# Optimization experiments

Hardware: AMD Instinct MI355X
Metric: run time of the kernel (lower is better)

The kernel has to match this reference:

```python
import jax, jax.numpy as jnp
import numpy as np

K = 16
CIN = 128
COUT = 128
EPS = 1e-5
SLOPE = 0.01  # default negative_slope of nn.LeakyReLU


def _bn(w, gamma, beta):
    # BatchNorm1d in training mode over channel axis (last): stats over (N, k)
    mean = jnp.mean(w, axis=(0, 1))
    var = jnp.var(w, axis=(0, 1))  # biased variance, as torch uses for normalization
    return (w - mean) * jax.lax.rsqrt(var + EPS) * gamma + beta


def _leaky(x):
    return jnp.where(x >= 0, x, SLOPE * x)


def setup_inputs() -> dict:
    key = jax.random.key(0)
    ks = jax.random.split(key, 10)
    N = 8192
    s = 0.05
    return {
        "fea_i": jax.random.normal(ks[0], (N, CIN), jnp.float32),
        "fea_last": jax.random.normal(ks[1], (N, CIN), jnp.float32),
        "xyz_i": jax.random.uniform(ks[2], (N, 3), jnp.float32),
        "xyz_last": jax.random.uniform(ks[3], (N, 3), jnp.float32),
        "batch": jnp.zeros((N,), jnp.int32),
        "Wq": jax.random.normal(ks[4], (COUT, CIN), jnp.float32) * s,
        "bq": jnp.zeros((COUT,), jnp.float32),
        "Wk": jax.random.normal(ks[5], (COUT, CIN), jnp.float32) * s,
        "bk": jnp.zeros((COUT,), jnp.float32),
        "Wv": jax.random.normal(ks[6], (COUT, CIN), jnp.float32) * s,
        "bv": jnp.zeros((COUT,), jnp.float32),
        "bn1_gamma": jnp.ones((COUT,), jnp.float32),
        "bn1_beta": jnp.zeros((COUT,), jnp.float32),
        "Wl": jax.random.normal(ks[7], (COUT, COUT), jnp.float32) * s,
        "bl": jnp.zeros((COUT,), jnp.float32),
        "bn2_gamma": jnp.ones((COUT,), jnp.float32),
        "bn2_beta": jnp.zeros((COUT,), jnp.float32),
    }


def reference(fea_i, fea_last, xyz_i, xyz_last, batch, Wq, bq, Wk, bk, Wv, bv,
              bn1_gamma, bn1_beta, Wl, bl, bn2_gamma, bn2_beta):
    # knn: for each point in xyz_last, K nearest neighbors in xyz_i (single batch)
    d2 = jnp.sum((xyz_last[:, None, :] - xyz_i[None, :, :]) ** 2, axis=-1)  # (N, N)
    _, idx = jax.lax.top_k(-d2, K)  # (N, K) indices into xyz_i / fea_i

    fk = fea_i[idx]                                   # (N, K, CIN) gathered neighbor feats
    q = fea_last @ Wq.T + bq                          # (N, COUT); fea_last[idx_last] == row-repeat
    kk = jnp.einsum('nkc,oc->nko', fk, Wk) + bk       # (N, K, COUT)
    w = q[:, None, :] - kk                            # (N, K, COUT)

    # lin_w: BN -> LeakyReLU -> Linear -> BN -> LeakyReLU
    w = _leaky(_bn(w, bn1_gamma, bn1_beta))
    w = jnp.einsum('nko,po->nkp', w, Wl) + bl
    w = _leaky(_bn(w, bn2_gamma, bn2_beta))

    w = jax.nn.softmax(w, axis=1)                     # softmax over K neighbors
    v = jnp.einsum('nkc,oc->nko', fk, Wv) + bv        # (N, K, COUT)
    return jnp.sum(w * v, axis=1)                     # (N, COUT)
```

## Files before the change

### kernel.cpp

```cpp
#include <hip/hip_runtime.h>
#include <stdint.h>

#define NPTS   8192
#define NROWS  (NPTS * 16)
#define SLOPE  0.01f
#define BN_EPS 1e-5f
#define INVM   (1.f / (float)NROWS)

#define TP     0.13f
#define TP2    (TP * TP)
#define LDEP   6
#define LSTR   7
#define TF     0.2f
#define TF2    0.04f
#define CAPF   408
#define EPSB   1e-5f

#define OFF_Q      0u
#define OFF_KP     4194304u
#define OFF_VP     8388608u
#define OFF_STATS  12582912u
#define OFF_TAB    12845056u
#define OFF_IDX    13041664u
#define OFF_BIG    13585408u
#define WS_NEED    47139840u

#define T_POFF 0

typedef __bf16 bf16x8 __attribute__((ext_vector_type(8)));
typedef float  f32x4  __attribute__((ext_vector_type(4)));

__device__ __forceinline__ unsigned int pack_bf2(float lo, float hi) {
  unsigned int a = __float_as_uint(lo);
  unsigned int b = __float_as_uint(hi);
  unsigned int ra = (a + 0x7fffu + ((a >> 16) & 1u)) >> 16;
  unsigned int rb = (b + 0x7fffu + ((b >> 16) & 1u)) & 0xffff0000u;
  return ra | rb;
}
__device__ __forceinline__ unsigned short bf1(float v) {
  unsigned int a = __float_as_uint(v);
  return (unsigned short)((a + 0x7fffu + ((a >> 16) & 1u)) >> 16);
}
__device__ __forceinline__ float bf2f(unsigned short u) {
  return __uint_as_float(((unsigned int)u) << 16);
}

__device__ __forceinline__ int cell_of(float x, float y, float z) {
  int cx = min(7, max(0, (int)(x * 8.f)));
  int cy = min(7, max(0, (int)(y * 8.f)));
  int cz = min(7, max(0, (int)(z * 8.f)));
  return (cz * 8 + cy) * 8 + cx;
}

__device__ __forceinline__ void insert16(unsigned long long* key, unsigned long long kk) {
  if (kk < key[15]) {
    #pragma unroll
    for (int u = 15; u >= 1; --u) {
      bool cm1 = kk < key[u - 1];
      bool cs  = kk < key[u];
      key[u] = cm1 ? key[u - 1] : (cs ? kk : key[u]);
    }
    key[0] = (kk < key[0]) ? kk : key[0];
  }
}

template<int D>
__device__ __forceinline__ void tournament16(unsigned long long (&lst)[D], int lane,
                                             int* __restrict__ sidxq, int* __restrict__ idxoq) {
  int myidx = 0;
  #pragma unroll 1
  for (int r = 0; r < 16; ++r) {
    const float hd = __uint_as_float((unsigned int)(lst[0] >> 32));
    float wm = hd;
    #pragma unroll
    for (int o = 32; o; o >>= 1) wm = fminf(wm, __shfl_xor(wm, o));
    bool iswin = (hd == wm);
    const unsigned long long wmask = __ballot(iswin);
    unsigned int widx;
    if (__popcll(wmask) > 1) {
      unsigned int mi = iswin ? (unsigned int)lst[0] : 0xffffffffu;
      #pragma unroll
      for (int o = 32; o; o >>= 1) {
        unsigned int u = (unsigned int)__shfl_xor((int)mi, o);
        mi = (u < mi) ? u : mi;
      }
      widx = mi;
      iswin = iswin && ((unsigned int)lst[0] == mi);
    } else {
      const int wl = (int)__builtin_ctzll(wmask);
      widx = (unsigned int)__builtin_amdgcn_readlane((int)(unsigned int)lst[0], wl);
    }
    #pragma unroll
    for (int u = 0; u < D - 1; ++u) lst[u] = iswin ? lst[u + 1] : lst[u];
    lst[D - 1] = iswin ? ~0ull : lst[D - 1];
    if (lane == r) myidx = (int)widx;
  }
  if (lane < 16) { idxoq[lane] = myidx; sidxq[lane] = myidx; }
}

template<int D>
__device__ __forceinline__ void extract_topk(const unsigned long long* __restrict__ poolq, int n, int lane,
                                             int* __restrict__ sidxq, int* __restrict__ idxoq) {
  unsigned long long lst[D];
  #pragma unroll
  for (int j = 0; j < D; ++j) lst[j] = ~0ull;
  for (int j = lane; j < n; j += 64) {
    unsigned long long kk = poolq[j];
    #pragma unroll
    for (int u = D - 1; u >= 1; --u) {
      bool cm1 = kk < lst[u - 1];
      bool cs  = kk < lst[u];
      lst[u] = cm1 ? lst[u - 1] : (cs ? kk : lst[u]);
    }
    lst[0] = (kk < lst[0]) ? kk : lst[0];
  }
  tournament16<D>(lst, lane, sidxq, idxoq);
}

__device__ __forceinline__ int scan_ball(const int* __restrict__ poff, const float4* __restrict__ bp,
                                         float qx, float qy, float qz, float rad, float r2, int cap,
                                         unsigned long long* __restrict__ poolw,
                                         int lane, unsigned long long below) {
  const int lx = max(0, (int)floorf((qx - rad - EPSB) * 8.f));
  const int hx = min(7, (int)floorf((qx + rad + EPSB) * 8.f));
  const int ly = max(0, (int)floorf((qy - rad - EPSB) * 8.f));
  const int hy = min(7, (int)floorf((qy + rad + EPSB) * 8.f));
  const int lz = max(0, (int)floorf((qz - rad - EPSB) * 8.f));
  const int hz = min(7, (int)floorf((qz + rad + EPSB) * 8.f));
  const int nrY = hy - ly + 1, nrows = nrY * (hz - lz + 1);
  int zi = 0;
  #pragma unroll
  for (int z2 = 1; z2 < 5; ++z2) zi += (lane >= z2 * nrY) ? 1 : 0;
  const int yi = lane - zi * nrY;
  int rs = 0, re = 0;
  if (lane < nrows) {
    const int crow = ((lz + zi) * 8 + (ly + yi)) * 8;
    rs = poff[crow + lx]; re = poff[crow + hx + 1];
  }
  int cnt = 0;
  for (int r = 0; r < nrows; ++r) {
    const int rsr = __builtin_amdgcn_readlane(rs, r);
    const int rer = __builtin_amdgcn_readlane(re, r);
    for (int base = rsr; base < rer; base += 64) {
      const int pos = base + lane;
      const float4 pp = bp[pos];
      float dx = qx - pp.x, dy = qy - pp.y, dz = qz - pp.z;
      float dd = fmaf(dx, dx, fmaf(dy, dy, dz * dz));
      bool g = (pos < rer) && (dd < r2);
      unsigned long long mask = __ballot(g);
      int p2 = cnt + (int)__popcll(mask & below);
      if (g && p2 < cap)
        poolw[p2] = ((unsigned long long)__float_as_uint(dd) << 32) | (unsigned int)__float_as_int(pp.w);
      cnt += (int)__popcll(mask);
    }
  }
  return cnt;
}

__global__ __launch_bounds__(1024) void k_bin(const float* __restrict__ xyz_i,
                                              int* __restrict__ tab,
                                              float* __restrict__ stats,
                                              float4* __restrict__ bp) {
  __shared__ int cnt[512];
  __shared__ int scn[512];
  const int t = threadIdx.x;
  #pragma unroll
  for (int i = 0; i < 8; ++i) stats[i * 1024 + t] = 0.f;
  if (t < 512) cnt[t] = 0;
  if (t < 64)  bp[NPTS + t] = make_float4(1e9f, 1e9f, 1e9f, __int_as_float(0));
  __syncthreads();

  float xs[8], ys[8], zs[8]; int cl[8];
  #pragma unroll
  for (int i = 0; i < 8; ++i) {
    const int p = i * 1024 + t;
    xs[i] = xyz_i[p * 3]; ys[i] = xyz_i[p * 3 + 1]; zs[i] = xyz_i[p * 3 + 2];
    cl[i] = cell_of(xs[i], ys[i], zs[i]);
    atomicAdd(&cnt[cl[i]], 1);
  }
  __syncthreads();

  if (t < 512) scn[t] = cnt[t];
  __syncthreads();
  for (int ofs = 1; ofs < 512; ofs <<= 1) {
    int add = (t < 512 && t >= ofs) ? scn[t - ofs] : 0;
    __syncthreads();
    if (t < 512) scn[t] += add;
    __syncthreads();
  }
  if (t < 512) tab[T_POFF + t] = scn[t] - cnt[t];
  if (t == 511) tab[T_POFF + 512] = scn[511];
  __syncthreads();
  if (t < 512) scn[t] -= cnt[t];
  __syncthreads();

  #pragma unroll
  for (int i = 0; i < 8; ++i) {
    const int pos = atomicAdd(&scn[cl[i]], 1);
    bp[pos] = make_float4(xs[i], ys[i], zs[i], __int_as_float(i * 1024 + t));
  }
}

__global__ __launch_bounds__(256) void k_proj(const float* __restrict__ fea_i,
                                              const float* __restrict__ fea_last,
                                              const float* __restrict__ Wq,
                                              const float* __restrict__ Wk,
                                              const float* __restrict__ Wv,
                                              const float* __restrict__ bq,
                                              const float* __restrict__ bk,
                                              const float* __restrict__ bv,
                                              float* __restrict__ Qo,
                                              float* __restrict__ Kpo,
                                              float* __restrict__ Vpo) {
  const int z = blockIdx.y;
  const float* A    = (z == 0) ? fea_last : fea_i;
  const float* W    = (z == 0) ? Wq : ((z == 1) ? Wk : Wv);
  const float* bias = (z == 0) ? bq : ((z == 1) ? bk : bv);
  float* Out        = (z == 0) ? Qo : ((z == 1) ? Kpo : Vpo);

  __shared__ unsigned short wl[128 * 128];
  const int t = threadIdx.x;
  const int lane = t & 63, w = t >> 6;

  #pragma unroll
  for (int i = 0; i < 8; ++i) {
    const int chunk = i * 256 + t;
    const int p = chunk >> 4, cseg = chunk & 15;
    const float4 wa = *(const float4*)(W + (size_t)p * 128 + cseg * 8);
    const float4 wb = *(const float4*)(W + (size_t)p * 128 + cseg * 8 + 4);
    uint4 pk;
    pk.x = pack_bf2(wa.x, wa.y); pk.y = pack_bf2(wa.z, wa.w);
    pk.z = pack_bf2(wb.x, wb.y); pk.w = pack_bf2(wb.z, wb.w);
    *(uint4*)((char*)wl + p * 256 + ((cseg * 16) ^ ((p & 7) << 4))) = pk;
  }
  __syncthreads();

  const int rowtile = blockIdx.x * 64 + w * 16;
  const int kslot = lane & 15, kgrp = lane >> 4;
  const float* Arow = A + (size_t)(rowtile + kslot) * 128;

  f32x4 acc[8];
  #pragma unroll
  for (int tt = 0; tt < 8; ++tt) acc[tt] = (f32x4){0.f, 0.f, 0.f, 0.f};

  #pragma unroll
  for (int s = 0; s < 4; ++s) {
    const int c0 = s * 32 + kgrp * 8;
    const float4 qa = *(const float4*)(Arow + c0);
    const float4 qb = *(const float4*)(Arow + c0 + 4);
    uint4 af;
    af.x = pack_bf2(qa.x, qa.y); af.y = pack_bf2(qa.z, qa.w);
    af.z = pack_bf2(qb.x, qb.y); af.w = pack_bf2(qb.z, qb.w);
    const bf16x8 Af = __builtin_bit_cast(bf16x8, af);
    const int cbyte = s * 64 + kgrp * 16;
    #pragma unroll
    for (int tt = 0; tt < 8; ++tt) {
      const int prow = tt * 16 + kslot;
      const uint4 bw = *(const uint4*)((const char*)wl + prow * 256 + (cbyte ^ ((prow & 7) << 4)));
      acc[tt] = __builtin_amdgcn_mfma_f32_16x16x32_bf16(Af, __builtin_bit_cast(bf16x8, bw), acc[tt], 0, 0, 0);
    }
  }

  #pragma unroll
  for (int tt = 0; tt < 8; ++tt) {
    const int col = tt * 16 + kslot;
    const float bb = bias[col];
    #pragma unroll
    for (int r = 0; r < 4; ++r) {
      const int row = rowtile + kgrp * 4 + r;
      Out[(size_t)row * 128 + col] = acc[tt][r] + bb;
    }
  }
}

__global__ __launch_bounds__(256) void k_knn(const int* __restrict__ tab,
                                             const float4* __restrict__ bp,
                                             const float* __restrict__ xyz_last,
                                             const float* __restrict__ Q,
                                             const float* __restrict__ Kp,
                                             int* __restrict__ idxo,
                                             float* __restrict__ st1) {
  __shared__ unsigned long long pool[4][64 * LSTR];
  __shared__ int sidx[4][16];
  __shared__ float red[4][256];
  const int t = threadIdx.x, lane = t & 63, wave = t >> 6;
  const int q = blockIdx.x * 4 + wave;
  const float qx = xyz_last[q * 3];
  const float qy = xyz_last[q * 3 + 1];
  const float qz = xyz_last[q * 3 + 2];
  const int* poff = &tab[T_POFF];
  const unsigned long long below = (1ull << lane) - 1ull;

  unsigned long long* myslots = &pool[wave][lane * LSTR];
  int cnt = 0;
  {
    const int lx = max(0, (int)floorf((qx - TP - EPSB) * 8.f));
    const int hx = min(7, (int)floorf((qx + TP + EPSB) * 8.f));
    const int ly = max(0, (int)floorf((qy - TP - EPSB) * 8.f));
    const int hy = min(7, (int)floorf((qy + TP + EPSB) * 8.f));
    const int lz = max(0, (int)floorf((qz - TP - EPSB) * 8.f));
    const int hz = min(7, (int)floorf((qz + TP + EPSB) * 8.f));
    const int nrY = hy - ly + 1, nrows = nrY * (hz - lz + 1);
    int zi = 0;
    #pragma unroll
    for (int z2 = 1; z2 < 5; ++z2) zi += (lane >= z2 * nrY) ? 1 : 0;
    const int yi = lane - zi * nrY;
    int rs = 0, re = 0;
    if (lane < nrows) {
      const int crow = ((lz + zi) * 8 + (ly + yi)) * 8;
      rs = poff[crow + lx]; re = poff[crow + hx + 1];
    }
    for (int r = 0; r < nrows; ++r) {
      const int rsr = __builtin_amdgcn_readlane(rs, r);
      const int rer = __builtin_amdgcn_readlane(re, r);
      #pragma unroll 2
      for (int base = rsr; base < rer; base += 64) {
        const int pos = base + lane;
        const float4 pp = bp[pos];
        float dx = qx - pp.x, dy = qy - pp.y, dz = qz - pp.z;
        float dd = fmaf(dx, dx, fmaf(dy, dy, dz * dz));
        if ((pos < rer) && (dd < TP2)) {
          if (cnt < LDEP)
            myslots[cnt] = ((unsigned long long)__float_as_uint(dd) << 32) | (unsigned int)__float_as_int(pp.w);
          ++cnt;
        }
      }
    }
  }
  const bool anyover = __ballot(cnt > LDEP) != 0ull;
  int tot = cnt;
  #pragma unroll
  for (int o = 32; o; o >>= 1) tot += __shfl_xor(tot, o);

  if (!anyover && tot >= 16) {
    unsigned long long lst[LDEP];
    #pragma unroll
    for (int j = 0; j < LDEP; ++j) lst[j] = ~0ull;
    for (int j = 0; j < cnt; ++j) {
      unsigned long long kk = myslots[j];
      #pragma unroll
      for (int u = LDEP - 1; u >= 1; --u) {
        bool cm1 = kk < lst[u - 1];
        bool cs  = kk < lst[u];
        lst[u] = cm1 ? lst[u - 1] : (cs ? kk : lst[u]);
      }
      lst[0] = (kk < lst[0]) ? kk : lst[0];
    }
    tournament16<LDEP>(lst, lane, &sidx[wave][0], &idxo[q * 16]);
  } else {
    unsigned long long* flat = &pool[wave][0];
    int c1 = scan_ball(poff, bp, qx, qy, qz, TF, TF2, CAPF, flat, lane, below);
    if (c1 >= 16 && c1 <= CAPF) {
      extract_topk<7>(flat, c1, lane, &sidx[wave][0], &idxo[q * 16]);
    } else {
      unsigned long long key[16];
      #pragma unroll
      for (int u = 0; u < 16; ++u) key[u] = ~0ull;
      for (int it = 0; it < NPTS / 64; ++it) {
        const float4 pp = bp[it * 64 + lane];
        float dx = qx - pp.x, dy = qy - pp.y, dz = qz - pp.z;
        float dd = fmaf(dx, dx, fmaf(dy, dy, dz * dz));
        insert16(key, ((unsigned long long)__float_as_uint(dd) << 32) | (unsigned int)__float_as_int(pp.w));
      }
      unsigned long long myout = ~0ull;
      #pragma unroll 1
      for (int r = 0; r < 16; ++r) {
        unsigned long long w = key[0];
        #pragma unroll
        for (int o = 32; o; o >>= 1) {
          unsigned long long u = __shfl_xor(w, o);
          w = (u < w) ? u : w;
        }
        if (key[0] == w) {
          #pragma unroll
          for (int u = 0; u < 15; ++u) key[u] = key[u + 1];
          key[15] = ~0ull;
        }
        if (lane == r) myout = w;
      }
      if (lane < 16) {
        idxo[q * 16 + lane] = (int)(myout & 0xffffffffull);
        sidx[wave][lane] = (int)(myout & 0xffffffffull);
      }
    }
  }

  const int c0 = lane * 2;
  const float2 qv = *(const float2*)(Q + (size_t)q * 128 + c0);
  float s0 = 0.f, s1 = 0.f, v0 = 0.f, v1 = 0.f;
  #pragma unroll 4
  for (int k = 0; k < 16; ++k) {
    const int pid = sidx[wave][k];
    const float2 kv = *(const float2*)(Kp + (size_t)pid * 128 + c0);
    const float w0 = qv.x - kv.x, w1 = qv.y - kv.y;
    s0 += w0; v0 += w0 * w0;
    s1 += w1; v1 += w1 * w1;
  }
  red[wave][c0]       = s0;  red[wave][c0 + 1]   = s1;
  red[wave][128 + c0] = v0;  red[wave][129 + c0] = v1;
  __syncthreads();
  {
    const float totv = red[0][t & 255] + red[1][t & 255] + red[2][t & 255] + red[3][t & 255];
    atomicAdd(&st1[(blockIdx.x & 15) * 256 + (t & 255)], totv);
  }
}

__global__ __launch_bounds__(256) void k_mid(const float* __restrict__ Q,
                                             const float* __restrict__ Kp,
                                             const int* __restrict__ idx,
                                             const float* __restrict__ Wl,
                                             const float* __restrict__ bl,
                                             const float* __restrict__ st1,
                                             const float* __restrict__ g1,
                                             const float* __restrict__ b1,
                                             float* __restrict__ stats2,
                                             unsigned short* __restrict__ Y) {
  __shared__ union {
    unsigned short wl[128 * 128];
    struct {
      unsigned short stage[64][136];
      float red[4 * 256];
    } ep;
  } sm;
  __shared__ float bn1s[256];

  const int t = threadIdx.x;
  const int lane = t & 63, w = t >> 6;
  const int rowbase = blockIdx.x * 64;

  #pragma unroll
  for (int i = 0; i < 8; ++i) {
    const int chunk = i * 256 + t;
    const int p = chunk >> 4, cseg = chunk & 15;
    const float4 wa = *(const float4*)(Wl + (size_t)p * 128 + cseg * 8);
    const float4 wb = *(const float4*)(Wl + (size_t)p * 128 + cseg * 8 + 4);
    uint4 pk;
    pk.x = pack_bf2(wa.x, wa.y); pk.y = pack_bf2(wa.z, wa.w);
    pk.z = pack_bf2(wb.x, wb.y); pk.w = pack_bf2(wb.z, wb.w);
    *(uint4*)((char*)sm.wl + p * 256 + ((cseg * 16) ^ ((p & 7) << 4))) = pk;
  }
  if (t < 128) {
    float s = 0.f, q2 = 0.f;
    #pragma unroll
    for (int r = 0; r < 16; ++r) { s += st1[r * 256 + t]; q2 += st1[r * 256 + 128 + t]; }
    const float mean = s * INVM;
    const float var  = fmaf(-mean, mean, q2 * INVM);
    const float sc = g1[t] * rsqrtf(var + BN_EPS);
    bn1s[t]       = sc;
    bn1s[128 + t] = fmaf(-mean, sc, b1[t]);
  }
  __syncthreads();

  const int n = blockIdx.x * 4 + w;
  const int kslot = lane & 15;
  const int kgrp  = lane >> 4;
  const int pid = idx[n * 16 + kslot];
  const float* Qrow = Q + (size_t)n * 128;
  const float* Krow = Kp + (size_t)pid * 128;

  f32x4 acc[8];
  #pragma unroll
  for (int tt = 0; tt < 8; ++tt) acc[tt] = (f32x4){0.f, 0.f, 0.f, 0.f};

  #pragma unroll
  for (int s = 0; s < 4; ++s) {
    const int c0 = s * 32 + kgrp * 8;
    const float4 qa = *(const float4*)(Qrow + c0);
    const float4 qb = *(const float4*)(Qrow + c0 + 4);
    const float4 ka = *(const float4*)(Krow + c0);
    const float4 kb = *(const float4*)(Krow + c0 + 4);
    const float4 sa = *(const float4*)(bn1s + c0);
    const float4 sb = *(const float4*)(bn1s + c0 + 4);
    const float4 ha = *(const float4*)(bn1s + 128 + c0);
    const float4 hb = *(const float4*)(bn1s + 128 + c0 + 4);
    float x[8];
    x[0] = fmaf(qa.x - ka.x, sa.x, ha.x);
    x[1] = fmaf(qa.y - ka.y, sa.y, ha.y);
    x[2] = fmaf(qa.z - ka.z, sa.z, ha.z);
    x[3] = fmaf(qa.w - ka.w, sa.w, ha.w);
    x[4] = fmaf(qb.x - kb.x, sb.x, hb.x);
    x[5] = fmaf(qb.y - kb.y, sb.y, hb.y);
    x[6] = fmaf(qb.z - kb.z, sb.z, hb.z);
    x[7] = fmaf(qb.w - kb.w, sb.w, hb.w);
    uint4 af;
    af.x = pack_bf2(fmaxf(x[0], SLOPE * x[0]), fmaxf(x[1], SLOPE * x[1]));
    af.y = pack_bf2(fmaxf(x[2], SLOPE * x[2]), fmaxf(x[3], SLOPE * x[3]));
    af.z = pack_bf2(fmaxf(x[4], SLOPE * x[4]), fmaxf(x[5], SLOPE * x[5]));
    af.w = pack_bf2(fmaxf(x[6], SLOPE * x[6]), fmaxf(x[7], SLOPE * x[7]));
    const bf16x8 A = __builtin_bit_cast(bf16x8, af);
    const int cbyte = s * 64 + kgrp * 16;
    #pragma unroll
    for (int tt = 0; tt < 8; ++tt) {
      const int prow = tt * 16 + kslot;
      const uint4 bw = *(const uint4*)((const char*)sm.wl + prow * 256 + (cbyte ^ ((prow & 7) << 4)));
      acc[tt] = __builtin_amdgcn_mfma_f32_16x16x32_bf16(A, __builtin_bit_cast(bf16x8, bw), acc[tt], 0, 0, 0);
    }
  }
  __syncthreads();

  #pragma unroll
  for (int tt = 0; tt < 8; ++tt) {
    const int col = tt * 16 + kslot;
    const float bb = bl[col];
    float s = 0.f, q2 = 0.f;
    #pragma unroll
    for (int r = 0; r < 4; ++r) {
      const float v = acc[tt][r] + bb;
      s += v; q2 += v * v;
      sm.ep.stage[w * 16 + kgrp * 4 + r][col] = bf1(v);
    }
    s  += __shfl_xor(s, 16);  s  += __shfl_xor(s, 32);
    q2 += __shfl_xor(q2, 16); q2 += __shfl_xor(q2, 32);
    if (kgrp == 0) {
      sm.ep.red[w * 256 + col]       = s;
      sm.ep.red[w * 256 + 128 + col] = q2;
    }
  }
  __syncthreads();

  #pragma unroll
  for (int i = 0; i < 4; ++i) {
    const int chunk = i * 256 + t;
    const int row = chunk >> 4, cc = chunk & 15;
    const uint4 v = *(const uint4*)&sm.ep.stage[row][cc * 8];
    *(uint4*)&Y[(size_t)(rowbase + row) * 128 + cc * 8] = v;
  }
  {
    const float tot = sm.ep.red[t] + sm.ep.red[256 + t] + sm.ep.red[512 + t] + sm.ep.red[768 + t];
    atomicAdd(&stats2[(blockIdx.x & 15) * 256 + t], tot);
  }
}

__global__ __launch_bounds__(128) void k_epi(const unsigned short* __restrict__ Y,
                                             const float* __restrict__ Vp,
                                             const int* __restrict__ idx,
                                             const float* __restrict__ st2,
                                             const float* __restrict__ g2,
                                             const float* __restrict__ b2,
                                             float* __restrict__ out) {
  const int n = blockIdx.x;
  const int p = threadIdx.x;
  float s = 0.f, q2 = 0.f;
  #pragma unroll
  for (int r = 0; r < 16; ++r) { s += st2[r * 256 + p]; q2 += st2[r * 256 + 128 + p]; }
  const float mean = s * INVM;
  const float var  = fmaf(-mean, mean, q2 * INVM);
  const float s2 = g2[p] * rsqrtf(var + BN_EPS);
  const float sh2 = fmaf(-mean, s2, b2[p]);

  float z[16];
  #pragma unroll
  for (int k = 0; k < 16; ++k) {
    float yv = bf2f(Y[(size_t)(n * 16 + k) * 128 + p]);
    float v = fmaf(yv, s2, sh2);
    z[k] = (v >= 0.f) ? v : SLOPE * v;
  }
  float m = z[0];
  #pragma unroll
  for (int k = 1; k < 16; ++k) m = fmaxf(m, z[k]);
  float acc = 0.f, denom = 0.f;
  #pragma unroll
  for (int k = 0; k < 16; ++k) {
    float e = __expf(z[k] - m);
    denom += e;
    const int pid = idx[n * 16 + k];
    acc = fmaf(e, Vp[(size_t)pid * 128 + p], acc);
  }
  out[(size_t)n * 128 + p] = acc / denom;
}

extern "C" void kernel_launch(void* const* d_in, const int* in_sizes, int n_in,
                              void* d_out, int out_size, void* d_ws, size_t ws_size,
                              hipStream_t stream) {
  const float* fea_i    = (const float*)d_in[0];
  const float* fea_last = (const float*)d_in[1];
  const float* xyz_i    = (const float*)d_in[2];
  const float* xyz_last = (const float*)d_in[3];
  const float* Wq = (const float*)d_in[5];
  const float* bq = (const float*)d_in[6];
  const float* Wk = (const float*)d_in[7];
  const float* bk = (const float*)d_in[8];
  const float* Wv = (const float*)d_in[9];
  const float* bv = (const float*)d_in[10];
  const float* g1 = (const float*)d_in[11];
  const float* b1 = (const float*)d_in[12];
  const float* Wl = (const float*)d_in[13];
  const float* bl = (const float*)d_in[14];
  const float* g2 = (const float*)d_in[15];
  const float* b2 = (const float*)d_in[16];

  if (ws_size < (size_t)WS_NEED) return;

  char* ws = (char*)d_ws;
  float*  Q      = (float*)(ws + OFF_Q);
  float*  Kp     = (float*)(ws + OFF_KP);
  float*  Vp     = (float*)(ws + OFF_VP);
  int*    tab    = (int*)  (ws + OFF_TAB);
  int*    idxb   = (int*)  (ws + OFF_IDX);
  float*  st1    = (float*)(ws + OFF_STATS);
  float*  st2    = st1 + 4096;
  float4* bp     = (float4*)(ws + OFF_BIG);
  unsigned short* Y = (unsigned short*)(ws + OFF_BIG);

  k_bin<<<1, 1024, 0, stream>>>(xyz_i, tab, st1, bp);
  k_proj<<<dim3(128, 3), 256, 0, stream>>>(fea_i, fea_last, Wq, Wk, Wv, bq, bk, bv, Q, Kp, Vp);
  k_knn<<<2048, 256, 0, stream>>>(tab, bp, xyz_last, Q, Kp, idxb, st1);
  k_mid<<<2048, 256, 0, stream>>>(Q, Kp, idxb, Wl, bl, st1, g1, b1, st2, Y);
  k_epi<<<8192, 128, 0, stream>>>(Y, Vp, idxb, st2, g2, b2, (float*)d_out);
}
```

Measured before the change: 104.3 us.

## Recompute Linear in output kernel instead of storing Y; fold binning into projection

The second-layer activations Y are no longer written to and re-read from global memory. A stats-only pass computes BN2 statistics, then a fused output kernel recomputes the MFMA Linear, applies BN2, LeakyReLU and the softmax-weighted V sum in one launch. The single-block binning kernel is also merged into the projection launch as an extra grid row, removing one launch and letting it overlap with the GEMMs. In exchange the Linear matmul and K gather run twice, and the binning block now uses 256 threads instead of 1024, which could lengthen the critical path of that grid.

Result: slower. 114.4 us (+9.7%).

```diff
diff --git a/kernel.cpp b/kernel.cpp
--- a/kernel.cpp
+++ b/kernel.cpp
@@ -36,13 +36,6 @@
   unsigned int ra = (a + 0x7fffu + ((a >> 16) & 1u)) >> 16;
   unsigned int rb = (b + 0x7fffu + ((b >> 16) & 1u)) & 0xffff0000u;
   return ra | rb;
-}
-__device__ __forceinline__ unsigned short bf1(float v) {
-  unsigned int a = __float_as_uint(v);
-  return (unsigned short)((a + 0x7fffu + ((a >> 16) & 1u)) >> 16);
-}
-__device__ __forceinline__ float bf2f(unsigned short u) {
-  return __uint_as_float(((unsigned int)u) << 16);
 }
 
 __device__ __forceinline__ int cell_of(float x, float y, float z) {
@@ -157,50 +150,6 @@
   return cnt;
 }
 
-__global__ __launch_bounds__(1024) void k_bin(const float* __restrict__ xyz_i,
-                                              int* __restrict__ tab,
-                                              float* __restrict__ stats,
-                                              float4* __restrict__ bp) {
-  __shared__ int cnt[512];
-  __shared__ int scn[512];
-  const int t = threadIdx.x;
-  #pragma unroll
-  for (int i = 0; i < 8; ++i) stats[i * 1024 + t] = 0.f;
-  if (t < 512) cnt[t] = 0;
-  if (t < 64)  bp[NPTS + t] = make_float4(1e9f, 1e9f, 1e9f, __int_as_float(0));
-  __syncthreads();
-
-  float xs[8], ys[8], zs[8]; int cl[8];
-  #pragma unroll
-  for (int i = 0; i < 8; ++i) {
-    const int p = i * 1024 + t;
-    xs[i] = xyz_i[p * 3]; ys[i] = xyz_i[p * 3 + 1]; zs[i] = xyz_i[p * 3 + 2];
-    cl[i] = cell_of(xs[i], ys[i], zs[i]);
-    atomicAdd(&cnt[cl[i]], 1);
-  }
-  __syncthreads();
-
-  if (t < 512) scn[t] = cnt[t];
-  __syncthreads();
-  for (int ofs = 1; ofs < 512; ofs <<= 1) {
-    int add = (t < 512 && t >= ofs) ? scn[t - ofs] : 0;
-    __syncthreads();
-    if (t < 512) scn[t] += add;
-    __syncthreads();
-  }
-  if (t < 512) tab[T_POFF + t] = scn[t] - cnt[t];
-  if (t == 511) tab[T_POFF + 512] = scn[511];
-  __syncthreads();
-  if (t < 512) scn[t] -= cnt[t];
-  __syncthreads();
-
-  #pragma unroll
-  for (int i = 0; i < 8; ++i) {
-    const int pos = atomicAdd(&scn[cl[i]], 1);
-    bp[pos] = make_float4(xs[i], ys[i], zs[i], __int_as_float(i * 1024 + t));
-  }
-}
-
 __global__ __launch_bounds__(256) void k_proj(const float* __restrict__ fea_i,
                                               const float* __restrict__ fea_last,
                                               const float* __restrict__ Wq,
@@ -209,17 +158,62 @@
                                               const float* __restrict__ bq,
                                               const float* __restrict__ bk,
                                               const float* __restrict__ bv,
+                                              const float* __restrict__ xyz_i,
+                                              int* __restrict__ tab,
+                                              float* __restrict__ stats,
+                                              float4* __restrict__ bp,
                                               float* __restrict__ Qo,
                                               float* __restrict__ Kpo,
                                               float* __restrict__ Vpo) {
+  __shared__ unsigned short wl[128 * 128];
+  const int t = threadIdx.x;
+
+  if (blockIdx.y == 3) {
+    if (blockIdx.x != 0) return;
+    int* cnt = (int*)wl;
+    int* sa  = cnt + 512;
+    int* sb  = sa + 512;
+    #pragma unroll
+    for (int i = 0; i < 32; ++i) stats[i * 256 + t] = 0.f;
+    cnt[t] = 0; cnt[t + 256] = 0;
+    if (t < 64) bp[NPTS + t] = make_float4(1e9f, 1e9f, 1e9f, __int_as_float(0));
+    __syncthreads();
+    #pragma unroll 4
+    for (int i = 0; i < 32; ++i) {
+      const int p = i * 256 + t;
+      atomicAdd(&cnt[cell_of(xyz_i[p * 3], xyz_i[p * 3 + 1], xyz_i[p * 3 + 2])], 1);
+    }
+    __syncthreads();
+    sa[t] = cnt[t]; sa[t + 256] = cnt[t + 256];
+    __syncthreads();
+    for (int ofs = 1; ofs < 512; ofs <<= 1) {
+      const int p1 = t + 256;
+      const int v0 = sa[t]  + ((t  >= ofs) ? sa[t  - ofs] : 0);
+      const int v1 = sa[p1] + ((p1 >= ofs) ? sa[p1 - ofs] : 0);
+      __syncthreads();
+      sa[t] = v0; sa[p1] = v1;
+      __syncthreads();
+    }
+    tab[T_POFF + t]       = sa[t]       - cnt[t];
+    tab[T_POFF + 256 + t] = sa[256 + t] - cnt[256 + t];
+    if (t == 255) tab[T_POFF + 512] = sa[511];
+    sb[t] = sa[t] - cnt[t]; sb[t + 256] = sa[256 + t] - cnt[256 + t];
+    __syncthreads();
+    #pragma unroll 4
+    for (int i = 0; i < 32; ++i) {
+      const int p = i * 256 + t;
+      const float x = xyz_i[p * 3], y = xyz_i[p * 3 + 1], z = xyz_i[p * 3 + 2];
+      const int pos = atomicAdd(&sb[cell_of(x, y, z)], 1);
+      bp[pos] = make_float4(x, y, z, __int_as_float(p));
+    }
+    return;
+  }
+
   const int z = blockIdx.y;
   const float* A    = (z == 0) ? fea_last : fea_i;
   const float* W    = (z == 0) ? Wq : ((z == 1) ? Wk : Wv);
   const float* bias = (z == 0) ? bq : ((z == 1) ? bk : bv);
   float* Out        = (z == 0) ? Qo : ((z == 1) ? Kpo : Vpo);
-
-  __shared__ unsigned short wl[128 * 128];
-  const int t = threadIdx.x;
   const int lane = t & 63, w = t >> 6;
 
   #pragma unroll
@@ -405,7 +399,116 @@
   }
 }
 
-__global__ __launch_bounds__(256) void k_mid(const float* __restrict__ Q,
+#define MID_CORE(Q_, Kp_, idx_, Wl_, st1_, g1_, b1_, wlbuf, bn1buf, accv)                        \
+  {                                                                                              \
+    _Pragma("unroll")                                                                            \
+    for (int i = 0; i < 8; ++i) {                                                                \
+      const int chunk = i * 256 + t;                                                             \
+      const int p = chunk >> 4, cseg = chunk & 15;                                               \
+      const float4 wa = *(const float4*)(Wl_ + (size_t)p * 128 + cseg * 8);                      \
+      const float4 wb = *(const float4*)(Wl_ + (size_t)p * 128 + cseg * 8 + 4);                  \
+      uint4 pk;                                                                                  \
+      pk.x = pack_bf2(wa.x, wa.y); pk.y = pack_bf2(wa.z, wa.w);                                  \
+      pk.z = pack_bf2(wb.x, wb.y); pk.w = pack_bf2(wb.z, wb.w);                                  \
+      *(uint4*)((char*)wlbuf + p * 256 + ((cseg * 16) ^ ((p & 7) << 4))) = pk;                   \
+    }                                                                                            \
+    if (t < 128) {                                                                               \
+      float s = 0.f, q2 = 0.f;                                                                   \
+      _Pragma("unroll")                                                                          \
+      for (int r = 0; r < 16; ++r) { s += st1_[r * 256 + t]; q2 += st1_[r * 256 + 128 + t]; }    \
+      const float mean = s * INVM;                                                               \
+      const float var  = fmaf(-mean, mean, q2 * INVM);                                           \
+      const float sc = g1_[t] * rsqrtf(var + BN_EPS);                                            \
+      bn1buf[t]       = sc;                                                                      \
+      bn1buf[128 + t] = fmaf(-mean, sc, b1_[t]);                                                 \
+    }                                                                                            \
+    __syncthreads();                                                                             \
+    const int pidA = idx_[n * 16 + kslot];                                                       \
+    const float* Qrow = Q_ + (size_t)n * 128;                                                    \
+    const float* Krow = Kp_ + (size_t)pidA * 128;                                                \
+    _Pragma("unroll")                                                                            \
+    for (int s = 0; s < 4; ++s) {                                                                \
+      const int c0 = s * 32 + kgrp * 8;                                                          \
+      const float4 qa = *(const float4*)(Qrow + c0);                                             \
+      const float4 qb = *(const float4*)(Qrow + c0 + 4);                                         \
+      const float4 ka = *(const float4*)(Krow + c0);                                             \
+      const float4 kb = *(const float4*)(Krow + c0 + 4);                                         \
+      const float4 sa = *(const float4*)(bn1buf + c0);                                           \
+      const float4 sb = *(const float4*)(bn1buf + c0 + 4);                                       \
+      const float4 ha = *(const float4*)(bn1buf + 128 + c0);                                     \
+      const float4 hb = *(const float4*)(bn1buf + 128 + c0 + 4);                                 \
+      float x[8];                                                                                \
+      x[0] = fmaf(qa.x - ka.x, sa.x, ha.x);                                                      \
+      x[1] = fmaf(qa.y - ka.y, sa.y, ha.y);                                                      \
+      x[2] = fmaf(qa.z - ka.z, sa.z, ha.z);                                                      \
+      x[3] = fmaf(qa.w - ka.w, sa.w, ha.w);                                                      \
+      x[4] = fmaf(qb.x - kb.x, sb.x, hb.x);                                                      \
+      x[5] = fmaf(qb.y - kb.y, sb.y, hb.y);                                                      \
+      x[6] = fmaf(qb.z - kb.z, sb.z, hb.z);                                                      \
+      x[7] = fmaf(qb.w - kb.w, sb.w, hb.w);                                                      \
+      uint4 af;                                                                                  \
+      af.x = pack_bf2(fmaxf(x[0], SLOPE * x[0]), fmaxf(x[1], SLOPE * x[1]));                     \
+      af.y = pack_bf2(fmaxf(x[2], SLOPE * x[2]), fmaxf(x[3], SLOPE * x[3]));                     \
+      af.z = pack_bf2(fmaxf(x[4], SLOPE * x[4]), fmaxf(x[5], SLOPE * x[5]));                     \
+      af.w = pack_bf2(fmaxf(x[6], SLOPE * x[6]), fmaxf(x[7], SLOPE * x[7]));                     \
+      const bf16x8 Aa = __builtin_bit_cast(bf16x8, af);                                          \
+      const int cbyte = s * 64 + kgrp * 16;                                                      \
+      _Pragma("unroll")                                                                          \
+      for (int tt = 0; tt < 8; ++tt) {                                                           \
+        const int prow = tt * 16 + kslot;                                                        \
+        const uint4 bw = *(const uint4*)((const char*)wlbuf + prow * 256 + (cbyte ^ ((prow & 7) << 4))); \
+        accv[tt] = __builtin_amdgcn_mfma_f32_16x16x32_bf16(Aa, __builtin_bit_cast(bf16x8, bw), accv[tt], 0, 0, 0); \
+      }                                                                                          \
+    }                                                                                            \
+  }
+
+__global__ __launch_bounds__(256) void k_stat2(const float* __restrict__ Q,
+                                               const float* __restrict__ Kp,
+                                               const int* __restrict__ idx,
+                                               const float* __restrict__ Wl,
+                                               const float* __restrict__ bl,
+                                               const float* __restrict__ st1,
+                                               const float* __restrict__ g1,
+                                               const float* __restrict__ b1,
+                                               float* __restrict__ st2) {
+  __shared__ unsigned short wl[128 * 128];
+  __shared__ float bn1s[256];
+  __shared__ float red[4 * 256];
+  const int t = threadIdx.x;
+  const int lane = t & 63, w = t >> 6;
+  const int n = blockIdx.x * 4 + w;
+  const int kslot = lane & 15, kgrp = lane >> 4;
+
+  f32x4 acc[8];
+  #pragma unroll
+  for (int tt = 0; tt < 8; ++tt) acc[tt] = (f32x4){0.f, 0.f, 0.f, 0.f};
+  MID_CORE(Q, Kp, idx, Wl, st1, g1, b1, wl, bn1s, acc)
+
+  #pragma unroll
+  for (int tt = 0; tt < 8; ++tt) {
+    const int col = tt * 16 + kslot;
+    const float bb = bl[col];
+    float s = 0.f, q2 = 0.f;
+    #pragma unroll
+    for (int r = 0; r < 4; ++r) {
+      const float v = acc[tt][r] + bb;
+      s += v; q2 += v * v;
+    }
+    s  += __shfl_xor(s, 16);  s  += __shfl_xor(s, 32);
+    q2 += __shfl_xor(q2, 16); q2 += __shfl_xor(q2, 32);
+    if (kgrp == 0) {
+      red[w * 256 + col]       = s;
+      red[w * 256 + 128 + col] = q2;
+    }
+  }
+  __syncthreads();
+  {
+    const float tot = red[t] + red[256 + t] + red[512 + t] + red[768 + t];
+    atomicAdd(&st2[(blockIdx.x & 15) * 256 + t], tot);
+  }
+}
+
+__global__ __launch_bounds__(256) void k_out(const float* __restrict__ Q,
                                              const float* __restrict__ Kp,
                                              const int* __restrict__ idx,
                                              const float* __restrict__ Wl,
@@ -413,160 +516,71 @@
                                              const float* __restrict__ st1,
                                              const float* __restrict__ g1,
                                              const float* __restrict__ b1,
-                                             float* __restrict__ stats2,
-                                             unsigned short* __restrict__ Y) {
-  __shared__ union {
-    unsigned short wl[128 * 128];
-    struct {
-      unsigned short stage[64][136];
-      float red[4 * 256];
-    } ep;
-  } sm;
+                                             const float* __restrict__ st2,
+                                             const float* __restrict__ g2,
+                                             const float* __restrict__ b2,
+                                             const float* __restrict__ Vp,
+                                             float* __restrict__ out) {
+  __shared__ unsigned short wl[128 * 128];
   __shared__ float bn1s[256];
-
+  __shared__ float bn2s[256];
+  __shared__ float ostage[512];
   const int t = threadIdx.x;
   const int lane = t & 63, w = t >> 6;
-  const int rowbase = blockIdx.x * 64;
-
-  #pragma unroll
-  for (int i = 0; i < 8; ++i) {
-    const int chunk = i * 256 + t;
-    const int p = chunk >> 4, cseg = chunk & 15;
-    const float4 wa = *(const float4*)(Wl + (size_t)p * 128 + cseg * 8);
-    const float4 wb = *(const float4*)(Wl + (size_t)p * 128 + cseg * 8 + 4);
-    uint4 pk;
-    pk.x = pack_bf2(wa.x, wa.y); pk.y = pack_bf2(wa.z, wa.w);
-    pk.z = pack_bf2(wb.x, wb.y); pk.w = pack_bf2(wb.z, wb.w);
-    *(uint4*)((char*)sm.wl + p * 256 + ((cseg * 16) ^ ((p & 7) << 4))) = pk;
-  }
-  if (t < 128) {
+  const int n = blockIdx.x * 4 + w;
+  const int kslot = lane & 15, kgrp = lane >> 4;
+
+  if (t >= 128 && t < 256) {
+    const int o = t - 128;
     float s = 0.f, q2 = 0.f;
     #pragma unroll
-    for (int r = 0; r < 16; ++r) { s += st1[r * 256 + t]; q2 += st1[r * 256 + 128 + t]; }
+    for (int r = 0; r < 16; ++r) { s += st2[r * 256 + o]; q2 += st2[r * 256 + 128 + o]; }
     const float mean = s * INVM;
     const float var  = fmaf(-mean, mean, q2 * INVM);
-    const float sc = g1[t] * rsqrtf(var + BN_EPS);
-    bn1s[t]       = sc;
-    bn1s[128 + t] = fmaf(-mean, sc, b1[t]);
-  }
-  __syncthreads();
-
-  const int n = blockIdx.x * 4 + w;
-  const int kslot = lane & 15;
-  const int kgrp  = lane >> 4;
-  const int pid = idx[n * 16 + kslot];
-  const float* Qrow = Q + (size_t)n * 128;
-  const float* Krow = Kp + (size_t)pid * 128;
+    const float sc = g2[o] * rsqrtf(var + BN_EPS);
+    bn2s[o]       = sc;
+    bn2s[128 + o] = fmaf(-mean, sc, b2[o]);
+  }
 
   f32x4 acc[8];
   #pragma unroll
   for (int tt = 0; tt < 8; ++tt) acc[tt] = (f32x4){0.f, 0.f, 0.f, 0.f};
-
-  #pragma unroll
-  for (int s = 0; s < 4; ++s) {
-    const int c0 = s * 32 + kgrp * 8;
-    const float4 qa = *(const float4*)(Qrow + c0);
-    const float4 qb = *(const float4*)(Qrow + c0 + 4);
-    const float4 ka = *(const float4*)(Krow + c0);
-    const float4 kb = *(const float4*)(Krow + c0 + 4);
-    const float4 sa = *(const float4*)(bn1s + c0);
-    const float4 sb = *(const float4*)(bn1s + c0 + 4);
-    const float4 ha = *(const float4*)(bn1s + 128 + c0);
-    const float4 hb = *(const float4*)(bn1s + 128 + c0 + 4);
-    float x[8];
-    x[0] = fmaf(qa.x - ka.x, sa.x, ha.x);
-    x[1] = fmaf(qa.y - ka.y, sa.y, ha.y);
-    x[2] = fmaf(qa.z - ka.z, sa.z, ha.z);
-    x[3] = fmaf(qa.w - ka.w, sa.w, ha.w);
-    x[4] = fmaf(qb.x - kb.x, sb.x, hb.x);
-    x[5] = fmaf(qb.y - kb.y, sb.y, hb.y);
-    x[6] = fmaf(qb.z - kb.z, sb.z, hb.z);
-    x[7] = fmaf(qb.w - kb.w, sb.w, hb.w);
-    uint4 af;
-    af.x = pack_bf2(fmaxf(x[0], SLOPE * x[0]), fmaxf(x[1], SLOPE * x[1]));
-    af.y = pack_bf2(fmaxf(x[2], SLOPE * x[2]), fmaxf(x[3], SLOPE * x[3]));
-    af.z = pack_bf2(fmaxf(x[4], SLOPE * x[4]), fmaxf(x[5], SLOPE * x[5]));
-    af.w = pack_bf2(fmaxf(x[6], SLOPE * x[6]), fmaxf(x[7], SLOPE * x[7]));
-    const bf16x8 A = __builtin_bit_cast(bf16x8, af);
-    const int cbyte = s * 64 + kgrp * 16;
-    #pragma unroll
-    for (int tt = 0; tt < 8; ++tt) {
-      const int prow = tt * 16 + kslot;
-      const uint4 bw = *(const uint4*)((const char*)sm.wl + prow * 256 + (cbyte ^ ((prow & 7) << 4)));
-      acc[tt] = __builtin_amdgcn_mfma_f32_16x16x32_bf16(A, __builtin_bit_cast(bf16x8, bw), acc[tt], 0, 0, 0);
-    }
-  }
-  __syncthreads();
+  MID_CORE(Q, Kp, idx, Wl, st1, g1, b1, wl, bn1s, acc)
+
+  int pid4[4];
+  #pragma unroll
+  for (int r = 0; r < 4; ++r) pid4[r] = idx[n * 16 + kgrp * 4 + r];
 
   #pragma unroll
   for (int tt = 0; tt < 8; ++tt) {
     const int col = tt * 16 + kslot;
     const float bb = bl[col];
-    float s = 0.f, q2 = 0.f;
+    const float s2v = bn2s[col], sh2v = bn2s[128 + col];
+    float zv[4];
     #pragma unroll
     for (int r = 0; r < 4; ++r) {
-      const float v = acc[tt][r] + bb;
-      s += v; q2 += v * v;
-      sm.ep.stage[w * 16 + kgrp * 4 + r][col] = bf1(v);
-    }
-    s  += __shfl_xor(s, 16);  s  += __shfl_xor(s, 32);
-    q2 += __shfl_xor(q2, 16); q2 += __shfl_xor(q2, 32);
-    if (kgrp == 0) {
-      sm.ep.red[w * 256 + col]       = s;
-      sm.ep.red[w * 256 + 128 + col] = q2;
-    }
+      const float y = fmaf(acc[tt][r] + bb, s2v, sh2v);
+      zv[r] = (y >= 0.f) ? y : SLOPE * y;
+    }
+    float m = fmaxf(fmaxf(zv[0], zv[1]), fmaxf(zv[2], zv[3]));
+    m = fmaxf(m, __shfl_xor(m, 16));
+    m = fmaxf(m, __shfl_xor(m, 32));
+    float d = 0.f, va = 0.f;
+    #pragma unroll
+    for (int r = 0; r < 4; ++r) {
+      const float e = __expf(zv[r] - m);
+      d += e;
+      va = fmaf(e, Vp[(size_t)pid4[r] * 128 + col], va);
+    }
+    d  += __shfl_xor(d, 16);  d  += __shfl_xor(d, 32);
+    va += __shfl_xor(va, 16); va += __shfl_xor(va, 32);
+    if (kgrp == 0) ostage[w * 128 + col] = va / d;
   }
   __syncthreads();
-
-  #pragma unroll
-  for (int i = 0; i < 4; ++i) {
-    const int chunk = i * 256 + t;
-    const int row = chunk >> 4, cc = chunk & 15;
-    const uint4 v = *(const uint4*)&sm.ep.stage[row][cc * 8];
-    *(uint4*)&Y[(size_t)(rowbase + row) * 128 + cc * 8] = v;
-  }
   {
-    const float tot = sm.ep.red[t] + sm.ep.red[256 + t] + sm.ep.red[512 + t] + sm.ep.red[768 + t];
-    atomicAdd(&stats2[(blockIdx.x & 15) * 256 + t], tot);
-  }
-}
-
-__global__ __launch_bounds__(128) void k_epi(const unsigned short* __restrict__ Y,
-                                             const float* __restrict__ Vp,
-                                             const int* __restrict__ idx,
-                                             const float* __restrict__ st2,
-                                             const float* __restrict__ g2,
-                                             const float* __restrict__ b2,
-                                             float* __restrict__ out) {
-  const int n = blockIdx.x;
-  const int p = threadIdx.x;
-  float s = 0.f, q2 = 0.f;
-  #pragma unroll
-  for (int r = 0; r < 16; ++r) { s += st2[r * 256 + p]; q2 += st2[r * 256 + 128 + p]; }
-  const float mean = s * INVM;
-  const float var  = fmaf(-mean, mean, q2 * INVM);
-  const float s2 = g2[p] * rsqrtf(var + BN_EPS);
-  const float sh2 = fmaf(-mean, s2, b2[p]);
-
-  float z[16];
-  #pragma unroll
-  for (int k = 0; k < 16; ++k) {
-    float yv = bf2f(Y[(size_t)(n * 16 + k) * 128 + p]);
-    float v = fmaf(yv, s2, sh2);
-    z[k] = (v >= 0.f) ? v : SLOPE * v;
-  }
-  float m = z[0];
-  #pragma unroll
-  for (int k = 1; k < 16; ++k) m = fmaxf(m, z[k]);
-  float acc = 0.f, denom = 0.f;
-  #pragma unroll
-  for (int k = 0; k < 16; ++k) {
-    float e = __expf(z[k] - m);
-    denom += e;
-    const int pid = idx[n * 16 + k];
-    acc = fmaf(e, Vp[(size_t)pid * 128 + p], acc);
-  }
-  out[(size_t)n * 128 + p] = acc / denom;
+    const float2 v = *(const float2*)&ostage[t * 2];
+    *(float2*)&out[(size_t)blockIdx.x * 512 + t * 2] = v;
+  }
 }
 
 extern "C" void kernel_launch(void* const* d_in, const int* in_sizes, int n_in,
@@ -600,11 +614,10 @@
   float*  st1    = (float*)(ws + OFF_STATS);
   float*  st2    = st1 + 4096;
   float4* bp     = (float4*)(ws + OFF_BIG);
-  unsigned short* Y = (unsigned short*)(ws + OFF_BIG);
-
-  k_bin<<<1, 1024, 0, stream>>>(xyz_i, tab, st1, bp);
-  k_proj<<<dim3(128, 3), 256, 0, stream>>>(fea_i, fea_last, Wq, Wk, Wv, bq, bk, bv, Q, Kp, Vp);
+
+  k_proj<<<dim3(128, 4), 256, 0, stream>>>(fea_i, fea_last, Wq, Wk, Wv, bq, bk, bv,
+                                           xyz_i, tab, st1, bp, Q, Kp, Vp);
   k_knn<<<2048, 256, 0, stream>>>(tab, bp, xyz_last, Q, Kp, idxb, st1);
-  k_mid<<<2048, 256, 0, stream>>>(Q, Kp, idxb, Wl, bl, st1, g1, b1, st2, Y);
-  k_epi<<<8192, 128, 0, stream>>>(Y, Vp, idxb, st2, g2, b2, (float*)d_out);
-}
+  k_stat2<<<2048, 256, 0, stream>>>(Q, Kp, idxb, Wl, bl, st1, g1, b1, st2);
+  k_out<<<2048, 256, 0, stream>>>(Q, Kp, idxb, Wl, bl, st1, g1, b1, st2, g2, b2, Vp, (float*)d_out);
+}
```
